# Kernel optimization log

Hardware: AMD Instinct MI355X
Metric: run time of the kernel (lower is better)

The kernel has to match this reference:

```python
import math
import jax, jax.numpy as jnp
import numpy as np

D_MODEL = 4096
N_Q_HEADS = 32
N_KV_HEADS = 8
HEAD_DIM = D_MODEL // N_Q_HEADS  # 128
N_GROUPS = N_Q_HEADS // N_KV_HEADS  # 4
B, S = 1, 2048


def setup_inputs() -> dict:
    key = jax.random.key(0)
    k1, k2, k3, k4, k5 = jax.random.split(key, 5)
    scale = 1.0 / math.sqrt(D_MODEL)
    return {
        "x": jax.random.normal(k1, (B, S, D_MODEL), dtype=jnp.float32),
        "W_q": jax.random.normal(k2, (N_Q_HEADS * HEAD_DIM, D_MODEL), dtype=jnp.float32) * scale,
        "W_k": jax.random.normal(k3, (N_KV_HEADS * HEAD_DIM, D_MODEL), dtype=jnp.float32) * scale,
        "W_v": jax.random.normal(k4, (N_KV_HEADS * HEAD_DIM, D_MODEL), dtype=jnp.float32) * scale,
        "W_o": jax.random.normal(k5, (D_MODEL, D_MODEL), dtype=jnp.float32) * scale,
    }


def reference(x, W_q, W_k, W_v, W_o):
    Bsz, Sq, _ = x.shape
    # projections (nn.Linear, no bias): y = x @ W.T
    q = (x @ W_q.T).reshape(Bsz, Sq, N_Q_HEADS, HEAD_DIM).transpose(0, 2, 1, 3)   # [B,Hq,S,d]
    k = (x @ W_k.T).reshape(Bsz, Sq, N_KV_HEADS, HEAD_DIM).transpose(0, 2, 1, 3)  # [B,Hkv,S,d]
    v = (x @ W_v.T).reshape(Bsz, Sq, N_KV_HEADS, HEAD_DIM).transpose(0, 2, 1, 3)
    # physical KV head repeat (repeat_interleave over head dim)
    k_rep = jnp.repeat(k, N_GROUPS, axis=1)  # [B,Hq,S,d]
    v_rep = jnp.repeat(v, N_GROUPS, axis=1)
    scores = jnp.einsum("bhqd,bhkd->bhqk", q, k_rep) / math.sqrt(HEAD_DIM)
    attn = jax.nn.softmax(scores, axis=-1)  # no causal mask in the original
    out = jnp.einsum("bhqk,bhkd->bhqd", attn, v_rep)
    out = out.transpose(0, 2, 1, 3).reshape(Bsz, Sq, D_MODEL)
    out = out @ W_o.T
    # original returns first n_kv_heads slices of the REPEATED k/v as the "cache"
    return out, (k_rep[:, :N_KV_HEADS], v_rep[:, :N_KV_HEADS])
```

## Files before the change

kernel.cpp:

```cpp
#include <hip/hip_runtime.h>
#include <hip/hip_bf16.h>

typedef __bf16 bf16;
typedef float f32x4 __attribute__((ext_vector_type(4)));
typedef float f32x16 __attribute__((ext_vector_type(16)));
typedef bf16 bf16x8 __attribute__((ext_vector_type(8)));
typedef bf16 bf16x2 __attribute__((ext_vector_type(2)));
typedef unsigned u32x4 __attribute__((ext_vector_type(4)));

#define MFMA16(a,b,c) __builtin_amdgcn_mfma_f32_16x16x32_bf16((a),(b),(c),0,0,0)
#define MFMA32(a,b,c) __builtin_amdgcn_mfma_f32_32x32x16_bf16((a),(b),(c),0,0,0)

__device__ __forceinline__ void gload16(const void* g, void* l) {
    __builtin_amdgcn_global_load_lds((const __attribute__((address_space(1))) unsigned*)g,
                                     (__attribute__((address_space(3))) unsigned*)l, 16, 0, 0);
}

__device__ __forceinline__ unsigned pk(float lo, float hi) {
    bf16x2 t; t[0] = (bf16)lo; t[1] = (bf16)hi;
    return __builtin_bit_cast(unsigned, t);
}

__device__ __forceinline__ void cvt8(const float* __restrict__ in, bf16* __restrict__ out, int i) {
    const float4* p = (const float4*)in + (size_t)i * 2;
    float4 a = p[0], b = p[1];
    bf16x8 o;
    o[0]=(bf16)a.x; o[1]=(bf16)a.y; o[2]=(bf16)a.z; o[3]=(bf16)a.w;
    o[4]=(bf16)b.x; o[5]=(bf16)b.y; o[6]=(bf16)b.z; o[7]=(bf16)b.w;
    *((bf16x8*)out + i) = o;
}

__global__ __launch_bounds__(256) void cvt_all(const float* __restrict__ x, const float* __restrict__ wq,
                                               const float* __restrict__ wk, const float* __restrict__ wv,
                                               bf16* __restrict__ xb, bf16* __restrict__ wqkv) {
    int i = blockIdx.x * 256 + threadIdx.x;
    const float* src; bf16* dst; int n8;
    switch (blockIdx.y) {
        case 0: src = x;  dst = xb;                 n8 = 1048576; break;
        case 1: src = wq; dst = wqkv;               n8 = 2097152; break;
        case 2: src = wk; dst = wqkv + 16777216;    n8 = 524288;  break;
        default: src = wv; dst = wqkv + 20971520;   n8 = 524288;  break;
    }
    if (i < n8) cvt8(src, dst, i);
}

__global__ __launch_bounds__(256) void cvt_one(const float* __restrict__ in, bf16* __restrict__ out, int n8) {
    int i = blockIdx.x * 256 + threadIdx.x;
    if (i < n8) cvt8(in, out, i);
}

__device__ __forceinline__ void stage_tile_qkv(const bf16* __restrict__ A, const bf16* __restrict__ B,
                                               int K, int bm, int bn, int k0,
                                               bf16* As, bf16* Bs, int tid) {
#pragma unroll
    for (int i=0;i<4;++i) {
        int off = i*8192 + tid*16;
        int row = off >> 7;
        int cg  = (tid & 7) ^ (row & 7);
        gload16(A + (size_t)(bm+row)*K + k0 + cg*8, (char*)As + off);
    }
#pragma unroll
    for (int i=0;i<3;++i) {
        int off = i*8192 + tid*16;
        int row = off >> 7;
        int cg  = (tid & 7) ^ (row & 7);
        gload16(B + (size_t)(bn+row)*K + k0 + cg*8, (char*)Bs + off);
    }
}

__global__ __launch_bounds__(512, 2) void gemm_qkv(const bf16* __restrict__ A, const bf16* __restrict__ W,
                                                   bf16* __restrict__ C, float qscale) {
    __shared__ __align__(16) bf16 As[2*16384];
    __shared__ __align__(16) bf16 Bs[2*12288];
    const int tid = threadIdx.x, lane = tid & 63, wv = tid >> 6;
    const int wm = wv >> 2, wn = wv & 3;
    const int lr = lane & 15, ls = lane >> 4;

    int flat = blockIdx.y * 8 + blockIdx.x;
    int id = (flat & 7) * 32 + (flat >> 3);
    const int bm = (id & 7) * 256, bn = (id >> 3) * 192;
    const int K = 4096, nt = 64;

    f32x4 acc[8][3];
#pragma unroll
    for (int mm=0;mm<8;++mm)
#pragma unroll
        for (int nn=0;nn<3;++nn)
#pragma unroll
            for (int r=0;r<4;++r) acc[mm][nn][r] = 0.f;

    stage_tile_qkv(A, W, K, bm, bn, 0,  As,         Bs,         tid);
    stage_tile_qkv(A, W, K, bm, bn, 64, As + 16384, Bs + 12288, tid);

    for (int t = 0; t < nt; ++t) {
        const int cur = t & 1;
        bf16* AsC = As + cur * 16384;
        bf16* BsC = Bs + cur * 12288;

        if (t < nt - 1) asm volatile("s_waitcnt vmcnt(7)" ::: "memory");
        else            asm volatile("s_waitcnt vmcnt(0)" ::: "memory");
        __builtin_amdgcn_s_barrier();
        __builtin_amdgcn_sched_barrier(0);

        bf16x8 af0[8], bf0[3];
#pragma unroll
        for (int mm=0;mm<8;++mm) {
            int row = wm*128 + mm*16 + lr;
            af0[mm] = *(const bf16x8*)((char*)AsC + row*128 + ((ls ^ (row&7))<<4));
        }
#pragma unroll
        for (int nn=0;nn<3;++nn) {
            int row = wn*48 + nn*16 + lr;
            bf0[nn] = *(const bf16x8*)((char*)BsC + row*128 + ((ls ^ (row&7))<<4));
        }
        asm volatile("s_waitcnt lgkmcnt(0)" ::: "memory");
        __builtin_amdgcn_sched_barrier(0);
        __builtin_amdgcn_s_setprio(1);
#pragma unroll
        for (int mm=0;mm<8;++mm)
#pragma unroll
            for (int nn=0;nn<3;++nn) acc[mm][nn] = MFMA16(af0[mm], bf0[nn], acc[mm][nn]);
        __builtin_amdgcn_s_setprio(0);

        bf16x8 af1[8], bf1[3];
#pragma unroll
        for (int mm=0;mm<8;++mm) {
            int row = wm*128 + mm*16 + lr;
            af1[mm] = *(const bf16x8*)((char*)AsC + row*128 + (((4+ls) ^ (row&7))<<4));
        }
#pragma unroll
        for (int nn=0;nn<3;++nn) {
            int row = wn*48 + nn*16 + lr;
            bf1[nn] = *(const bf16x8*)((char*)BsC + row*128 + (((4+ls) ^ (row&7))<<4));
        }
        asm volatile("s_waitcnt lgkmcnt(0)" ::: "memory");
        __builtin_amdgcn_sched_barrier(0);
        __builtin_amdgcn_s_barrier();
        __builtin_amdgcn_sched_barrier(0);

        if (t + 2 < nt)
            stage_tile_qkv(A, W, K, bm, bn, (t+2) << 6, AsC, BsC, tid);

        __builtin_amdgcn_s_setprio(1);
#pragma unroll
        for (int mm=0;mm<8;++mm)
#pragma unroll
            for (int nn=0;nn<3;++nn) acc[mm][nn] = MFMA16(af1[mm], bf1[nn], acc[mm][nn]);
        __builtin_amdgcn_s_setprio(0);
    }

#pragma unroll
    for (int mm=0;mm<8;++mm)
#pragma unroll
        for (int nn=0;nn<3;++nn) {
            int ng = bn + wn*48 + nn*16 + lr;
            float s = (ng < 4096) ? qscale : 1.0f;
#pragma unroll
            for (int r=0;r<4;++r) {
                int mg = bm + wm*128 + mm*16 + ls*4 + r;
                C[(size_t)mg * 6144 + ng] = (bf16)(acc[mm][nn][r] * s);
            }
        }
}

__device__ __forceinline__ void stage_tile(const bf16* __restrict__ A, const bf16* __restrict__ B,
                                           int K, int bm, int bn, int k0,
                                           bf16* As, bf16* Bs, int wv, int lane) {
#pragma unroll
    for (int i=0;i<4;++i) {
        int off = i*4096 + wv*1024 + lane*16;
        int row = off >> 7;
        int cg = (lane & 7) ^ (row & 7);
        gload16(A + (size_t)(bm+row)*K + k0 + cg*8, (char*)As + off);
    }
#pragma unroll
    for (int i=0;i<4;++i) {
        int off = i*4096 + wv*1024 + lane*16;
        int row = off >> 7;
        int cg = (lane & 7) ^ (row & 7);
        gload16(B + (size_t)(bn+row)*K + k0 + cg*8, (char*)Bs + off);
    }
}

__device__ __forceinline__ void gemm_core(const bf16* __restrict__ A, const bf16* __restrict__ B,
                                          int K, int bm, int bn, bf16* As, bf16* Bs, f32x4 (&acc)[4][4]) {
    const int tid = threadIdx.x, lane = tid & 63, wv = tid >> 6;
    const int wr = wv >> 1, wc = wv & 1, lr = lane & 15, ls = lane >> 4;

#pragma unroll
    for (int mm=0;mm<4;++mm)
#pragma unroll
        for (int nn=0;nn<4;++nn)
#pragma unroll
            for (int r=0;r<4;++r) acc[mm][nn][r] = 0.f;

    const int nt = K >> 6;
    stage_tile(A, B, K, bm, bn, 0,  As,        Bs,        wv, lane);
    stage_tile(A, B, K, bm, bn, 64, As + 8192, Bs + 8192, wv, lane);

    for (int t = 0; t < nt; ++t) {
        const int cur = t & 1;
        bf16* AsC = As + cur * 8192;
        bf16* BsC = Bs + cur * 8192;

        if (t < nt - 1) asm volatile("s_waitcnt vmcnt(8)" ::: "memory");
        else            asm volatile("s_waitcnt vmcnt(0)" ::: "memory");
        __builtin_amdgcn_s_barrier();
        __builtin_amdgcn_sched_barrier(0);

        bf16x8 af[2][4], bfr[2][4];
#pragma unroll
        for (int ks=0; ks<2; ++ks) {
#pragma unroll
            for (int mm=0;mm<4;++mm) {
                int row = wr*64 + mm*16 + lr;
                af[ks][mm] = *(const bf16x8*)((char*)AsC + row*128 + (((ks*4+ls) ^ (row&7))<<4));
            }
#pragma unroll
            for (int nn=0;nn<4;++nn) {
                int row = wc*64 + nn*16 + lr;
                bfr[ks][nn] = *(const bf16x8*)((char*)BsC + row*128 + (((ks*4+ls) ^ (row&7))<<4));
            }
        }
        asm volatile("s_waitcnt lgkmcnt(0)" ::: "memory");
        __builtin_amdgcn_sched_barrier(0);
        __builtin_amdgcn_s_barrier();
        __builtin_amdgcn_sched_barrier(0);

        if (t + 2 < nt)
            stage_tile(A, B, K, bm, bn, (t+2) << 6, AsC, BsC, wv, lane);

        __builtin_amdgcn_s_setprio(1);
#pragma unroll
        for (int ks=0; ks<2; ++ks)
#pragma unroll
            for (int mm=0;mm<4;++mm)
#pragma unroll
                for (int nn=0;nn<4;++nn)
                    acc[mm][nn] = MFMA16(af[ks][mm], bfr[ks][nn], acc[mm][nn]);
        __builtin_amdgcn_s_setprio(0);
    }
}

__global__ __launch_bounds__(256) void gemm_o(const bf16* __restrict__ A, const bf16* __restrict__ B,
                                              float* __restrict__ Cp) {
    __shared__ __align__(16) bf16 As[2*128*64];
    __shared__ __align__(16) bf16 Bs[2*128*64];
    int flat = blockIdx.y * gridDim.x + blockIdx.x;
    int id = (flat & 7) * 64 + (flat >> 3);
    int bm = (id & 15) * 128, bn = (id >> 4) * 128;
    f32x4 acc[4][4];
    gemm_core(A, B, 4096, bm, bn, As, Bs, acc);

    const int lane = threadIdx.x & 63, wv = threadIdx.x >> 6;
    const int wr = wv >> 1, wc = wv & 1, lr = lane & 15, ls = lane >> 4;
#pragma unroll
    for (int mm=0;mm<4;++mm)
#pragma unroll
        for (int nn=0;nn<4;++nn)
#pragma unroll
            for (int r=0;r<4;++r) {
                int mg = bm + wr*64 + mm*16 + ls*4 + r;
                int ng = bn + wc*64 + nn*16 + lr;
                Cp[(size_t)mg * 4096 + ng] = acc[mm][nn][r];
            }
}

__global__ __launch_bounds__(256) void trans_cache(const bf16* __restrict__ QKVb, bf16* __restrict__ Vt,
                                                   float* __restrict__ cacheK, float* __restrict__ cacheV) {
    int b = blockIdx.x;
    if (b < 512) {
        __shared__ bf16 t[64][70];
        int dt = b & 15, st = b >> 4;
        int tt = threadIdx.x;
        int r = tt >> 2, c0 = (tt & 3) * 16;
#pragma unroll
        for (int i = 0; i < 2; ++i) {
            bf16x8 v = *(const bf16x8*)(QKVb + (size_t)(st*64 + r)*6144 + 5120 + dt*64 + c0 + i*8);
#pragma unroll
            for (int j = 0; j < 8; ++j) t[c0 + i*8 + j][r] = v[j];
        }
        __syncthreads();
        int c = tt >> 2, r0 = (tt & 3) * 16;
#pragma unroll
        for (int i = 0; i < 2; ++i) {
            bf16x8 v = *(const bf16x8*)(&t[c][r0 + i*8]);
            *(bf16x8*)(Vt + (size_t)(dt*64 + c)*2048 + st*64 + r0 + i*8) = v;
        }
    } else {
        int g = (b - 512) * 256 + threadIdx.x;
        int d8 = g & 15, s = (g >> 4) & 2047, j = (g >> 15) & 7, kv = g >> 18;
        int hk = j >> 2;
        bf16x8 v = *(const bf16x8*)(QKVb + (size_t)s*6144 + 4096 + kv*1024 + hk*128 + d8*8);
        float* dst = (kv ? cacheV : cacheK) + ((size_t)j*2048 + s)*128 + d8*8;
        float4 lo, hi;
        lo.x=(float)v[0]; lo.y=(float)v[1]; lo.z=(float)v[2]; lo.w=(float)v[3];
        hi.x=(float)v[4]; hi.y=(float)v[5]; hi.z=(float)v[6]; hi.w=(float)v[7];
        *(float4*)dst = lo;
        *(float4*)(dst + 4) = hi;
    }
}

__device__ __forceinline__ void stage_kv(const bf16* __restrict__ QKVb, const bf16* __restrict__ Vt,
                                         char* Ks, char* Vs, int kvh, int kt, int buf,
                                         int wv, int lane) {
#pragma unroll
    for (int i=0;i<2;++i) {
        int off = i*8192 + wv*1024 + lane*16;
        int row = off >> 8;
        int cg = (lane & 15) ^ (row & 7);
        gload16(QKVb + (size_t)(kt*64+row)*6144 + 4096 + kvh*128 + cg*8, Ks + buf*16384 + i*8192 + wv*1024);
    }
#pragma unroll
    for (int i=0;i<2;++i) {
        int off = i*8192 + wv*1024 + lane*16;
        int d = off >> 7;
        int cg = (lane & 7) ^ (d & 7);
        gload16(Vt + (size_t)(kvh*128+d)*2048 + kt*64 + cg*8, Vs + buf*16384 + i*8192 + wv*1024);
    }
}

__global__ __launch_bounds__(512) void flash_attn(const bf16* __restrict__ QKVb, const bf16* __restrict__ Vt,
                                                  bf16* __restrict__ AO) {
    __shared__ __align__(16) char Ks[2*16384];
    __shared__ __align__(16) char Vs[2*16384];
    const int tid = threadIdx.x, lane = tid & 63, wq = tid >> 6;
    const int l31 = lane & 31, hi = lane >> 5;
    const int h = blockIdx.y, kvh = h >> 2;
    const int q0w = blockIdx.x * 256 + wq * 32;

    bf16x8 qf[8];
#pragma unroll
    for (int f=0; f<8; ++f)
        qf[f] = *(const bf16x8*)(QKVb + (size_t)(q0w + l31)*6144 + h*128 + f*16 + hi*8);

    f32x16 acc[4];
#pragma unroll
    for (int db=0;db<4;++db)
#pragma unroll
        for (int r=0;r<16;++r) acc[db][r] = 0.f;
    float mrun = -1e30f, lrun = 0.f;

    stage_kv(QKVb, Vt, Ks, Vs, kvh, 0, 0, wq, lane);
    __syncthreads();

    for (int t = 0; t < 32; ++t) {
        const int cur = t & 1;
        if (t + 1 < 32) stage_kv(QKVb, Vt, Ks, Vs, kvh, t+1, cur^1, wq, lane);

        const char* KsB = Ks + cur*16384;
        f32x16 sc[2];
#pragma unroll
        for (int kc=0;kc<2;++kc)
#pragma unroll
            for (int r=0;r<16;++r) sc[kc][r] = 0.f;
        __builtin_amdgcn_s_setprio(1);
#pragma unroll
        for (int f=0; f<8; ++f) {
            int r0 = l31, r1 = 32 + l31;
            bf16x8 k0 = *(const bf16x8*)(KsB + r0*256 + (((f*2+hi) ^ (r0&7))<<4));
            bf16x8 k1 = *(const bf16x8*)(KsB + r1*256 + (((f*2+hi) ^ (r1&7))<<4));
            sc[0] = MFMA32(k0, qf[f], sc[0]);
            sc[1] = MFMA32(k1, qf[f], sc[1]);
        }
        __builtin_amdgcn_s_setprio(0);

        float tmax = sc[0][0];
#pragma unroll
        for (int r=1;r<16;++r) tmax = fmaxf(tmax, sc[0][r]);
#pragma unroll
        for (int r=0;r<16;++r) tmax = fmaxf(tmax, sc[1][r]);
        tmax = fmaxf(tmax, __shfl_xor(tmax, 32, 64));
        if (!__all(tmax <= mrun + 8.f)) {
            float mnew = fmaxf(mrun, tmax);
            float corr = __expf(mrun - mnew);
            mrun = mnew;
            lrun *= corr;
#pragma unroll
            for (int r=0;r<16;++r) {
                float cr = __shfl(corr, (r&3) + 8*(r>>2) + 4*hi, 64);
#pragma unroll
                for (int db=0;db<4;++db) acc[db][r] *= cr;
            }
        }
        float rs = 0.f;
#pragma unroll
        for (int kc=0;kc<2;++kc)
#pragma unroll
            for (int r=0;r<16;++r) { float e = __expf(sc[kc][r] - mrun); sc[kc][r] = e; rs += e; }
        rs += __shfl_xor(rs, 32, 64);
        lrun += rs;

        bf16x8 pa[4];
#pragma unroll
        for (int kb=0;kb<4;++kb) {
            const int kc = kb>>1, r0 = (kb&1)*8;
            unsigned a0 = pk(sc[kc][r0+0], sc[kc][r0+1]);
            unsigned a1 = pk(sc[kc][r0+2], sc[kc][r0+3]);
            unsigned b0 = pk(sc[kc][r0+4], sc[kc][r0+5]);
            unsigned b1 = pk(sc[kc][r0+6], sc[kc][r0+7]);
            unsigned sa0 = (unsigned)__shfl_xor((int)a0, 32, 64);
            unsigned sa1 = (unsigned)__shfl_xor((int)a1, 32, 64);
            unsigned sb0 = (unsigned)__shfl_xor((int)b0, 32, 64);
            unsigned sb1 = (unsigned)__shfl_xor((int)b1, 32, 64);
            u32x4 w;
            w[0] = hi ? sb0 : a0;
            w[1] = hi ? sb1 : a1;
            w[2] = hi ? b0 : sa0;
            w[3] = hi ? b1 : sa1;
            pa[kb] = __builtin_bit_cast(bf16x8, w);
        }

        const char* VsB = Vs + cur*16384;
        __builtin_amdgcn_s_setprio(1);
#pragma unroll
        for (int db=0;db<4;++db) {
            const int d = db*32 + l31;
#pragma unroll
            for (int kb=0;kb<4;++kb) {
                bf16x8 vf = *(const bf16x8*)(VsB + d*128 + (((kb*2+hi) ^ (d&7))<<4));
                acc[db] = MFMA32(pa[kb], vf, acc[db]);
            }
        }
        __builtin_amdgcn_s_setprio(0);
        __syncthreads();
    }

    float linv = 1.0f / lrun;
#pragma unroll
    for (int r=0;r<16;++r) {
        int crw = (r&3) + 8*(r>>2) + 4*hi;
        float lv = __shfl(linv, crw, 64);
        size_t qrow = (size_t)q0w + crw;
#pragma unroll
        for (int db=0;db<4;++db)
            AO[qrow*4096 + h*128 + db*32 + l31] = (bf16)(acc[db][r] * lv);
    }
}

extern "C" void kernel_launch(void* const* d_in, const int* in_sizes, int n_in,
                              void* d_out, int out_size, void* d_ws, size_t ws_size,
                              hipStream_t stream) {
    const float* x  = (const float*)d_in[0];
    const float* Wq = (const float*)d_in[1];
    const float* Wk = (const float*)d_in[2];
    const float* Wv = (const float*)d_in[3];
    const float* Wo = (const float*)d_in[4];

    bf16* xb   = (bf16*)d_ws;
    bf16* QKVb = xb + (size_t)8388608;
    bf16* Wqkv = QKVb + (size_t)12582912;
    bf16* Vt  = xb;
    bf16* Wob = Wqkv;
    bf16* AO  = Wqkv + (size_t)16777216;

    float* out = (float*)d_out;
    float* cacheK = out + (size_t)8388608;
    float* cacheV = cacheK + (size_t)2097152;

    const float qscale = 0.08838834764831845f;

    cvt_all<<<dim3(8192, 4), 256, 0, stream>>>(x, Wq, Wk, Wv, xb, Wqkv);
    gemm_qkv<<<dim3(8, 32), 512, 0, stream>>>(xb, Wqkv, QKVb, qscale);
    cvt_one<<<8192, 256, 0, stream>>>(Wo, Wob, 2097152);
    trans_cache<<<2560, 256, 0, stream>>>(QKVb, Vt, cacheK, cacheV);
    flash_attn<<<dim3(8, 32), 512, 0, stream>>>(QKVb, Vt, AO);
    gemm_o<<<dim3(16, 32), 256, 0, stream>>>(AO, Wob, out);
}
```

Measured before the change: 307.6 us.

## Double KV tile to 128 keys in flash attention and fuse Wo conversion launch

Flash attention now stages 128 keys per iteration instead of 64, using 128KB of LDS double-buffered, so the loop runs 16 times with half as many barriers and softmax-rescale checks. The P·V loop now builds each P fragment just before its MFMAs, so the pa array is no longer kept live across the loop. Separately, the W_o fp32-to-bf16 conversion is merged into the cache/transpose kernel to drop one launch. The larger LDS footprint limits occupancy to one block per CU and raises register pressure from the larger score array.

```diff
diff --git a/kernel.cpp b/kernel.cpp
--- a/kernel.cpp
+++ b/kernel.cpp
@@ -44,11 +44,6 @@
     if (i < n8) cvt8(src, dst, i);
 }
 
-__global__ __launch_bounds__(256) void cvt_one(const float* __restrict__ in, bf16* __restrict__ out, int n8) {
-    int i = blockIdx.x * 256 + threadIdx.x;
-    if (i < n8) cvt8(in, out, i);
-}
-
 __device__ __forceinline__ void stage_tile_qkv(const bf16* __restrict__ A, const bf16* __restrict__ B,
                                                int K, int bm, int bn, int k0,
                                                bf16* As, bf16* Bs, int tid) {
@@ -266,8 +261,9 @@
             }
 }
 
-__global__ __launch_bounds__(256) void trans_cache(const bf16* __restrict__ QKVb, bf16* __restrict__ Vt,
-                                                   float* __restrict__ cacheK, float* __restrict__ cacheV) {
+__global__ __launch_bounds__(256) void trans_cache_cvt(const bf16* __restrict__ QKVb, bf16* __restrict__ Vt,
+                                                       float* __restrict__ cacheK, float* __restrict__ cacheV,
+                                                       const float* __restrict__ Wo, bf16* __restrict__ Wob) {
     int b = blockIdx.x;
     if (b < 512) {
         __shared__ bf16 t[64][70];
@@ -287,7 +283,7 @@
             bf16x8 v = *(const bf16x8*)(&t[c][r0 + i*8]);
             *(bf16x8*)(Vt + (size_t)(dt*64 + c)*2048 + st*64 + r0 + i*8) = v;
         }
-    } else {
+    } else if (b < 2560) {
         int g = (b - 512) * 256 + threadIdx.x;
         int d8 = g & 15, s = (g >> 4) & 2047, j = (g >> 15) & 7, kv = g >> 18;
         int hk = j >> 2;
@@ -298,32 +294,35 @@
         hi.x=(float)v[4]; hi.y=(float)v[5]; hi.z=(float)v[6]; hi.w=(float)v[7];
         *(float4*)dst = lo;
         *(float4*)(dst + 4) = hi;
+    } else {
+        int i = (b - 2560) * 256 + threadIdx.x;
+        if (i < 2097152) cvt8(Wo, Wob, i);
     }
 }
 
 __device__ __forceinline__ void stage_kv(const bf16* __restrict__ QKVb, const bf16* __restrict__ Vt,
                                          char* Ks, char* Vs, int kvh, int kt, int buf,
-                                         int wv, int lane) {
-#pragma unroll
-    for (int i=0;i<2;++i) {
-        int off = i*8192 + wv*1024 + lane*16;
+                                         int tid) {
+#pragma unroll
+    for (int i=0;i<4;++i) {
+        int off = i*8192 + tid*16;
         int row = off >> 8;
-        int cg = (lane & 15) ^ (row & 7);
-        gload16(QKVb + (size_t)(kt*64+row)*6144 + 4096 + kvh*128 + cg*8, Ks + buf*16384 + i*8192 + wv*1024);
-    }
-#pragma unroll
-    for (int i=0;i<2;++i) {
-        int off = i*8192 + wv*1024 + lane*16;
-        int d = off >> 7;
-        int cg = (lane & 7) ^ (d & 7);
-        gload16(Vt + (size_t)(kvh*128+d)*2048 + kt*64 + cg*8, Vs + buf*16384 + i*8192 + wv*1024);
+        int cg = (tid & 15) ^ (row & 7);
+        gload16(QKVb + (size_t)(kt*128+row)*6144 + 4096 + kvh*128 + cg*8, Ks + buf*32768 + off);
+    }
+#pragma unroll
+    for (int i=0;i<4;++i) {
+        int off = i*8192 + tid*16;
+        int d = off >> 8;
+        int cg = (tid & 15) ^ (d & 7);
+        gload16(Vt + (size_t)(kvh*128+d)*2048 + kt*128 + cg*8, Vs + buf*32768 + off);
     }
 }
 
 __global__ __launch_bounds__(512) void flash_attn(const bf16* __restrict__ QKVb, const bf16* __restrict__ Vt,
                                                   bf16* __restrict__ AO) {
-    __shared__ __align__(16) char Ks[2*16384];
-    __shared__ __align__(16) char Vs[2*16384];
+    __shared__ __align__(16) char Ks[2*32768];
+    __shared__ __align__(16) char Vs[2*32768];
     const int tid = threadIdx.x, lane = tid & 63, wq = tid >> 6;
     const int l31 = lane & 31, hi = lane >> 5;
     const int h = blockIdx.y, kvh = h >> 2;
@@ -341,35 +340,36 @@
         for (int r=0;r<16;++r) acc[db][r] = 0.f;
     float mrun = -1e30f, lrun = 0.f;
 
-    stage_kv(QKVb, Vt, Ks, Vs, kvh, 0, 0, wq, lane);
+    stage_kv(QKVb, Vt, Ks, Vs, kvh, 0, 0, tid);
     __syncthreads();
 
-    for (int t = 0; t < 32; ++t) {
+    for (int t = 0; t < 16; ++t) {
         const int cur = t & 1;
-        if (t + 1 < 32) stage_kv(QKVb, Vt, Ks, Vs, kvh, t+1, cur^1, wq, lane);
-
-        const char* KsB = Ks + cur*16384;
-        f32x16 sc[2];
-#pragma unroll
-        for (int kc=0;kc<2;++kc)
+        if (t + 1 < 16) stage_kv(QKVb, Vt, Ks, Vs, kvh, t+1, cur^1, tid);
+
+        const char* KsB = Ks + cur*32768;
+        f32x16 sc[4];
+#pragma unroll
+        for (int kc=0;kc<4;++kc)
 #pragma unroll
             for (int r=0;r<16;++r) sc[kc][r] = 0.f;
         __builtin_amdgcn_s_setprio(1);
 #pragma unroll
         for (int f=0; f<8; ++f) {
-            int r0 = l31, r1 = 32 + l31;
-            bf16x8 k0 = *(const bf16x8*)(KsB + r0*256 + (((f*2+hi) ^ (r0&7))<<4));
-            bf16x8 k1 = *(const bf16x8*)(KsB + r1*256 + (((f*2+hi) ^ (r1&7))<<4));
-            sc[0] = MFMA32(k0, qf[f], sc[0]);
-            sc[1] = MFMA32(k1, qf[f], sc[1]);
+#pragma unroll
+            for (int kc=0;kc<4;++kc) {
+                int row = kc*32 + l31;
+                bf16x8 kf = *(const bf16x8*)(KsB + row*256 + (((f*2+hi) ^ (row&7))<<4));
+                sc[kc] = MFMA32(kf, qf[f], sc[kc]);
+            }
         }
         __builtin_amdgcn_s_setprio(0);
 
         float tmax = sc[0][0];
 #pragma unroll
-        for (int r=1;r<16;++r) tmax = fmaxf(tmax, sc[0][r]);
-#pragma unroll
-        for (int r=0;r<16;++r) tmax = fmaxf(tmax, sc[1][r]);
+        for (int kc=0;kc<4;++kc)
+#pragma unroll
+            for (int r=0;r<16;++r) tmax = fmaxf(tmax, sc[kc][r]);
         tmax = fmaxf(tmax, __shfl_xor(tmax, 32, 64));
         if (!__all(tmax <= mrun + 8.f)) {
             float mnew = fmaxf(mrun, tmax);
@@ -385,15 +385,16 @@
         }
         float rs = 0.f;
 #pragma unroll
-        for (int kc=0;kc<2;++kc)
+        for (int kc=0;kc<4;++kc)
 #pragma unroll
             for (int r=0;r<16;++r) { float e = __expf(sc[kc][r] - mrun); sc[kc][r] = e; rs += e; }
         rs += __shfl_xor(rs, 32, 64);
         lrun += rs;
 
-        bf16x8 pa[4];
-#pragma unroll
-        for (int kb=0;kb<4;++kb) {
+        const char* VsB = Vs + cur*32768;
+        __builtin_amdgcn_s_setprio(1);
+#pragma unroll
+        for (int kb=0;kb<8;++kb) {
             const int kc = kb>>1, r0 = (kb&1)*8;
             unsigned a0 = pk(sc[kc][r0+0], sc[kc][r0+1]);
             unsigned a1 = pk(sc[kc][r0+2], sc[kc][r0+3]);
@@ -408,18 +409,12 @@
             w[1] = hi ? sb1 : a1;
             w[2] = hi ? b0 : sa0;
             w[3] = hi ? b1 : sa1;
-            pa[kb] = __builtin_bit_cast(bf16x8, w);
-        }
-
-        const char* VsB = Vs + cur*16384;
-        __builtin_amdgcn_s_setprio(1);
-#pragma unroll
-        for (int db=0;db<4;++db) {
-            const int d = db*32 + l31;
-#pragma unroll
-            for (int kb=0;kb<4;++kb) {
-                bf16x8 vf = *(const bf16x8*)(VsB + d*128 + (((kb*2+hi) ^ (d&7))<<4));
-                acc[db] = MFMA32(pa[kb], vf, acc[db]);
+            bf16x8 pa = __builtin_bit_cast(bf16x8, w);
+#pragma unroll
+            for (int db=0;db<4;++db) {
+                const int d = db*32 + l31;
+                bf16x8 vf = *(const bf16x8*)(VsB + d*256 + (((kb*2+hi) ^ (d&7))<<4));
+                acc[db] = MFMA32(pa, vf, acc[db]);
             }
         }
         __builtin_amdgcn_s_setprio(0);
@@ -462,8 +457,7 @@
 
     cvt_all<<<dim3(8192, 4), 256, 0, stream>>>(x, Wq, Wk, Wv, xb, Wqkv);
     gemm_qkv<<<dim3(8, 32), 512, 0, stream>>>(xb, Wqkv, QKVb, qscale);
-    cvt_one<<<8192, 256, 0, stream>>>(Wo, Wob, 2097152);
-    trans_cache<<<2560, 256, 0, stream>>>(QKVb, Vt, cacheK, cacheV);
+    trans_cache_cvt<<<10752, 256, 0, stream>>>(QKVb, Vt, cacheK, cacheV, Wo, Wob);
     flash_attn<<<dim3(8, 32), 512, 0, stream>>>(QKVb, Vt, AO);
     gemm_o<<<dim3(16, 32), 256, 0, stream>>>(AO, Wob, out);
 }
```

After: 298.6 us. -2.9%, faster.
